# Kernel optimization log

Measured on AMD Instinct MI355X. Metric: run time of the kernel, lower is better.

The kernel has to match this reference:

```python
import jax, jax.numpy as jnp
import numpy as np

NUM_TOKENS = 16384
HIDDEN = 2048
HEAD_SIZE = 128
NUM_HEADS = 16
NUM_KV_HEADS = 4
NUM_EXPERTS = 4
QKV_OUT = (NUM_HEADS + 2 * NUM_KV_HEADS) * HEAD_SIZE  # 3072


def setup_inputs() -> dict:
    key = jax.random.key(0)
    k_x, k_m, k_w = jax.random.split(key, 3)
    x = jax.random.normal(k_x, (NUM_TOKENS, HIDDEN), dtype=jnp.float32)
    # tokens are pre-grouped by modality (dispatcher splits contiguously)
    modality_mapping = jnp.sort(
        jax.random.randint(k_m, (NUM_TOKENS,), 0, NUM_EXPERTS, dtype=jnp.int32)
    )
    # per-expert QKV weight, layout [E, out_features, in_features] like nn.Linear
    W = jax.random.normal(k_w, (NUM_EXPERTS, QKV_OUT, HIDDEN), dtype=jnp.float32) * 0.02
    return {"x": x, "W": W, "modality_mapping": modality_mapping}


def reference(x, W, modality_mapping):
    # Per-modality-group dense QKV projection, then concat back in order.
    # Since groups are contiguous in token order, this equals a masked sum
    # over the (small, fixed) expert set: out[t] = x[t] @ W[id[t]].T
    num_experts = W.shape[0]
    out = jnp.zeros((x.shape[0], W.shape[1]), dtype=x.dtype)
    for e in range(num_experts):  # small fixed loop over experts
        mask = (modality_mapping == e)[:, None]
        xe = jnp.where(mask, x, 0.0)  # zero out tokens not in this group
        out = out + jnp.einsum("td,od->to", xe, W[e])
    return out
```

## Files before the change

### kernel.cpp

```cpp
#include <hip/hip_runtime.h>
#include <hip/hip_bf16.h>
#include <stdint.h>

typedef unsigned short u16;
typedef __attribute__((ext_vector_type(8))) short bf16x8;
typedef __attribute__((ext_vector_type(4))) float f32x4;

#define TOKENS   16384
#define HIDDEN   2048
#define QKV_OUT  3072
#define NEXP     4

#define BM 128
#define BN 128
#define BK 64
#define RT_TILES (TOKENS / BM)
#define CT_TILES (QKV_OUT / BN)


__device__ __forceinline__ uint32_t f2bf(float f) {
  uint32_t u = __builtin_bit_cast(uint32_t, f);
  return (u + 0x7FFFu + ((u >> 16) & 1u)) >> 16;
}

__global__ void cvt_f32_to_bf16(const float* __restrict__ in,
                                u16* __restrict__ out, long n8) {
  long i0 = (long)blockIdx.x * blockDim.x + threadIdx.x;
  long stride = (long)gridDim.x * blockDim.x;
  for (long p = i0; p < n8; p += stride) {
    const float4* s = (const float4*)in + p * 2;
    float4 a = s[0], b = s[1];
    uint4 q;
    q.x = f2bf(a.x) | (f2bf(a.y) << 16);
    q.y = f2bf(a.z) | (f2bf(a.w) << 16);
    q.z = f2bf(b.x) | (f2bf(b.y) << 16);
    q.w = f2bf(b.z) | (f2bf(b.w) << 16);
    ((uint4*)out)[p] = q;
  }
}


typedef const __attribute__((address_space(1))) void* gptr_t;
typedef __attribute__((address_space(3))) void* lptr_t;

__device__ __forceinline__ void gload16(const u16* g, u16* lds) {
  __builtin_amdgcn_global_load_lds((gptr_t)g, (lptr_t)lds, 16, 0, 0);
}


__global__ void moe_qkv_gemm(const u16* __restrict__ Xb,
                             const u16* __restrict__ Wb,
                             const int* __restrict__ mm,
                             float* __restrict__ out) {
  __shared__ u16 As[BM * BK];
  __shared__ u16 Bs[BN * BK];

  const int nwg = RT_TILES * CT_TILES;
  const int cpx = nwg >> 3;
  int bid = blockIdx.x;
  int swz = (bid & 7) * cpx + (bid >> 3);
  const int rt = swz / CT_TILES;
  const int ct = swz % CT_TILES;

  const int row0 = rt * BM;
  const int col0 = ct * BN;

  const int tid  = threadIdx.x;
  const int lane = tid & 63;
  const int wid  = tid >> 6;
  const int wr   = wid >> 1;
  const int wc   = wid & 1;

  const int e_lo = mm[row0];
  const int e_hi = mm[row0 + BM - 1];

  f32x4 acc[4][4];
#pragma unroll
  for (int m = 0; m < 4; ++m)
#pragma unroll
    for (int n = 0; n < 4; ++n) acc[m][n] = (f32x4){0.f, 0.f, 0.f, 0.f};

  const int srow = wid * 8 + (lane >> 3);
  const int scol = (lane & 7) * 8;

  auto compute_tile = [&]() {
#pragma unroll
    for (int kk = 0; kk < BK; kk += 32) {
      bf16x8 af[4], bfr[4];
#pragma unroll
      for (int m = 0; m < 4; ++m)
        af[m] = *(const bf16x8*)&As[(wr * 64 + m * 16 + (lane & 15)) * BK + kk + (lane >> 4) * 8];
#pragma unroll
      for (int n = 0; n < 4; ++n)
        bfr[n] = *(const bf16x8*)&Bs[(wc * 64 + n * 16 + (lane & 15)) * BK + kk + (lane >> 4) * 8];
#pragma unroll
      for (int m = 0; m < 4; ++m)
#pragma unroll
        for (int n = 0; n < 4; ++n)
          acc[m][n] = __builtin_amdgcn_mfma_f32_16x16x32_bf16(af[m], bfr[n], acc[m][n], 0, 0, 0);
    }
  };

  if (e_lo == e_hi) {
    const u16* We   = Wb + (size_t)e_lo * QKV_OUT * HIDDEN;
    const u16* Arow = Xb + (size_t)row0 * HIDDEN;
    const u16* Brow = We + (size_t)col0 * HIDDEN;
    for (int kt = 0; kt < HIDDEN; kt += BK) {
#pragma unroll
      for (int i = 0; i < 4; ++i) {
        gload16(Arow + (size_t)(i * 32 + srow) * HIDDEN + kt + scol, &As[i * 2048 + wid * 512]);
        gload16(Brow + (size_t)(i * 32 + srow) * HIDDEN + kt + scol, &Bs[i * 2048 + wid * 512]);
      }
      __syncthreads();
      compute_tile();
      __syncthreads();
    }
  } else {
    for (int e = e_lo; e <= e_hi; ++e) {
      const u16* We   = Wb + (size_t)e * QKV_OUT * HIDDEN;
      const u16* Brow = We + (size_t)col0 * HIDDEN;
      bool keep[4];
#pragma unroll
      for (int i = 0; i < 4; ++i) keep[i] = (mm[row0 + i * 32 + srow] == e);
      for (int kt = 0; kt < HIDDEN; kt += BK) {
#pragma unroll
        for (int i = 0; i < 4; ++i) {
          uint4 v = make_uint4(0u, 0u, 0u, 0u);
          if (keep[i])
            v = *(const uint4*)&Xb[(size_t)(row0 + i * 32 + srow) * HIDDEN + kt + scol];
          *(uint4*)&As[(i * 32 + srow) * BK + scol] = v;
          gload16(Brow + (size_t)(i * 32 + srow) * HIDDEN + kt + scol, &Bs[i * 2048 + wid * 512]);
        }
        __syncthreads();
        compute_tile();
        __syncthreads();
      }
    }
  }

#pragma unroll
  for (int m = 0; m < 4; ++m)
#pragma unroll
    for (int n = 0; n < 4; ++n) {
      f32x4 c = acc[m][n];
      int r0 = row0 + wr * 64 + m * 16 + (lane >> 4) * 4;
      int cc = col0 + wc * 64 + n * 16 + (lane & 15);
#pragma unroll
      for (int j = 0; j < 4; ++j)
        out[(size_t)(r0 + j) * QKV_OUT + cc] = c[j];
    }
}


extern "C" void kernel_launch(void* const* d_in, const int* in_sizes, int n_in,
                              void* d_out, int out_size, void* d_ws, size_t ws_size,
                              hipStream_t stream) {
  const float* x  = (const float*)d_in[0];
  const float* W  = (const float*)d_in[1];
  const int*   mm = (const int*)d_in[2];
  float* out = (float*)d_out;

  u16* Xb = (u16*)d_ws;
  u16* Wb = Xb + (size_t)TOKENS * HIDDEN;

  const long nx8 = (long)TOKENS * HIDDEN / 8;
  const long nw8 = (long)NEXP * QKV_OUT * HIDDEN / 8;
  cvt_f32_to_bf16<<<2048, 256, 0, stream>>>(x, Xb, nx8);
  cvt_f32_to_bf16<<<2048, 256, 0, stream>>>(W, Wb, nw8);

  moe_qkv_gemm<<<RT_TILES * CT_TILES, 256, 0, stream>>>(Xb, Wb, mm, out);
}
```

Measured before the change: 683.9 us.

## XOR-swizzle LDS tile layout and merge bf16 conversion kernels into one launch

Changes the LDS layout of the A and B tiles to an XOR swizzle of the 16-byte chunk index by row, so MFMA fragment reads avoid bank conflicts. The global source columns are permuted so the direct global-to-LDS loads land in swizzled positions, and the masked path writes into the swizzled slot directly. The two f32-to-bf16 conversion kernels are also merged into a single one-element-per-thread launch. This trades a slightly more complex addressing scheme for fewer LDS bank conflicts and one less kernel launch.

```diff
diff --git a/kernel.cpp b/kernel.cpp
--- a/kernel.cpp
+++ b/kernel.cpp
@@ -23,20 +23,23 @@
   return (u + 0x7FFFu + ((u >> 16) & 1u)) >> 16;
 }
 
-__global__ void cvt_f32_to_bf16(const float* __restrict__ in,
-                                u16* __restrict__ out, long n8) {
-  long i0 = (long)blockIdx.x * blockDim.x + threadIdx.x;
-  long stride = (long)gridDim.x * blockDim.x;
-  for (long p = i0; p < n8; p += stride) {
-    const float4* s = (const float4*)in + p * 2;
-    float4 a = s[0], b = s[1];
-    uint4 q;
-    q.x = f2bf(a.x) | (f2bf(a.y) << 16);
-    q.y = f2bf(a.z) | (f2bf(a.w) << 16);
-    q.z = f2bf(b.x) | (f2bf(b.y) << 16);
-    q.w = f2bf(b.z) | (f2bf(b.w) << 16);
-    ((uint4*)out)[p] = q;
-  }
+#define NX8 ((long)TOKENS * HIDDEN / 8)
+#define NW8 ((long)NEXP * QKV_OUT * HIDDEN / 8)
+
+__global__ void cvt_all(const float* __restrict__ x, const float* __restrict__ W,
+                        u16* __restrict__ Xb, u16* __restrict__ Wb) {
+  long gid = (long)blockIdx.x * blockDim.x + threadIdx.x;
+  const float* src; u16* dst; long p;
+  if (gid < NX8) { src = x;  dst = Xb; p = gid; }
+  else           { src = W;  dst = Wb; p = gid - NX8; }
+  const float4* s = (const float4*)src + p * 2;
+  float4 a = s[0], b = s[1];
+  uint4 q;
+  q.x = f2bf(a.x) | (f2bf(a.y) << 16);
+  q.y = f2bf(a.z) | (f2bf(a.w) << 16);
+  q.z = f2bf(b.x) | (f2bf(b.y) << 16);
+  q.w = f2bf(b.z) | (f2bf(b.w) << 16);
+  ((uint4*)dst)[p] = q;
 }
 
 
@@ -45,6 +48,10 @@
 
 __device__ __forceinline__ void gload16(const u16* g, u16* lds) {
   __builtin_amdgcn_global_load_lds((gptr_t)g, (lptr_t)lds, 16, 0, 0);
+}
+
+__device__ __forceinline__ int lds_u16(int row, int chunk) {
+  return row * BK + ((chunk ^ (row & 7)) << 3);
 }
 
 
@@ -80,19 +87,21 @@
 #pragma unroll
     for (int n = 0; n < 4; ++n) acc[m][n] = (f32x4){0.f, 0.f, 0.f, 0.f};
 
-  const int srow = wid * 8 + (lane >> 3);
-  const int scol = (lane & 7) * 8;
+  const int srow  = wid * 8 + (lane >> 3);
+  const int schk  = (lane & 7) ^ ((lane >> 3) & 7);
+  const int scol  = schk << 3;
 
   auto compute_tile = [&]() {
 #pragma unroll
-    for (int kk = 0; kk < BK; kk += 32) {
+    for (int kk = 0; kk < 2; ++kk) {
+      const int chunk = kk * 4 + (lane >> 4);
       bf16x8 af[4], bfr[4];
 #pragma unroll
       for (int m = 0; m < 4; ++m)
-        af[m] = *(const bf16x8*)&As[(wr * 64 + m * 16 + (lane & 15)) * BK + kk + (lane >> 4) * 8];
+        af[m] = *(const bf16x8*)&As[lds_u16(wr * 64 + m * 16 + (lane & 15), chunk)];
 #pragma unroll
       for (int n = 0; n < 4; ++n)
-        bfr[n] = *(const bf16x8*)&Bs[(wc * 64 + n * 16 + (lane & 15)) * BK + kk + (lane >> 4) * 8];
+        bfr[n] = *(const bf16x8*)&Bs[lds_u16(wc * 64 + n * 16 + (lane & 15), chunk)];
 #pragma unroll
       for (int m = 0; m < 4; ++m)
 #pragma unroll
@@ -128,7 +137,7 @@
           uint4 v = make_uint4(0u, 0u, 0u, 0u);
           if (keep[i])
             v = *(const uint4*)&Xb[(size_t)(row0 + i * 32 + srow) * HIDDEN + kt + scol];
-          *(uint4*)&As[(i * 32 + srow) * BK + scol] = v;
+          *(uint4*)&As[(i * 32 + srow) * BK + ((lane & 7) << 3)] = v;
           gload16(Brow + (size_t)(i * 32 + srow) * HIDDEN + kt + scol, &Bs[i * 2048 + wid * 512]);
         }
         __syncthreads();
@@ -163,10 +172,8 @@
   u16* Xb = (u16*)d_ws;
   u16* Wb = Xb + (size_t)TOKENS * HIDDEN;
 
-  const long nx8 = (long)TOKENS * HIDDEN / 8;
-  const long nw8 = (long)NEXP * QKV_OUT * HIDDEN / 8;
-  cvt_f32_to_bf16<<<2048, 256, 0, stream>>>(x, Xb, nx8);
-  cvt_f32_to_bf16<<<2048, 256, 0, stream>>>(W, Wb, nw8);
+  const long ntot8 = NX8 + NW8;
+  cvt_all<<<(int)(ntot8 / 256), 256, 0, stream>>>(x, W, Xb, Wb);
 
   moe_qkv_gemm<<<RT_TILES * CT_TILES, 256, 0, stream>>>(Xb, Wb, mm, out);
 }
```

New measurement: 652.7 us. -4.6%, faster.
